# Kernel tuning notes

Measured on AMD Instinct MI355X. Metric: run time of the kernel, lower is better.

## Reference

```python
import jax, jax.numpy as jnp
import numpy as np

R, C = 9, 9  # local window (rows, cols)


def setup_inputs() -> dict:
    key = jax.random.key(0)
    k1, k2, k3, k4, k5 = jax.random.split(key, 5)
    q = jax.random.normal(k1, (8, 256, 128, 128), jnp.float32)      # (B, q_size, H, W)
    c_t = jax.random.normal(k2, (8, 256, 512), jnp.float32)          # (B, T, c_size)
    W_a = jax.random.normal(k3, (512, 256), jnp.float32) * 0.04      # Linear(q_size -> c_size), no bias
    W_p = jax.random.normal(k4, (256, 512), jnp.float32) * 0.04      # Linear(c_size -> p_size)
    V_p = jax.random.normal(k5, (2, 256), jnp.float32) * 0.06        # Linear(p_size -> 2)
    return {"q": q, "c_t": c_t, "W_a": W_a, "W_p": W_p, "V_p": V_p}


def reference(q, c_t, W_a, W_p, V_p):
    B, D, H, W = q.shape
    T = c_t.shape[1]
    S = H  # q.size(2) before padding

    # predictive alignment: p_t = S * sigmoid(V_p(tanh(W_p(c_t))))  -> (B, T, 2)
    p_t = S * jax.nn.sigmoid(jnp.tanh(c_t @ W_p.T) @ V_p.T)

    # pad top/left with NaN, flatten spatial dims
    qp = jnp.pad(q, ((0, 0), (0, 0), (1, 0), (1, 0)), constant_values=jnp.nan)
    rows, cols = H + 1, W + 1
    qf = qp.reshape(B, D, rows * cols).transpose(0, 2, 1)  # (B, rows*cols, D)

    roff = jnp.arange(-(R // 2), (R + 1) // 2)  # R offsets
    coff = jnp.arange(-(C // 2), (C + 1) // 2)  # C offsets
    r = jnp.clip(jnp.round(p_t[..., 0]).astype(jnp.int32)[..., None] + roff + 1, 0, rows) % rows  # (B,T,R)
    c = jnp.clip(jnp.round(p_t[..., 1]).astype(jnp.int32)[..., None] + coff + 1, 0, cols) % cols  # (B,T,C)

    # flat window indices, order i*C + j (matches torch stack order)
    s = (r[..., :, None] * cols + c[..., None, :]).reshape(B, T, R * C)

    # gather windows: (B, T, R*C, D)
    qg = jnp.take_along_axis(qf, s.reshape(B, T * R * C, 1), axis=1).reshape(B, T, R * C, D)
    nan_loc = jnp.isnan(qg[..., 0])                    # (B, T, R*C)
    qg = jnp.where(nan_loc[..., None], 0.0, qg)

    # Gaussian positional weighting
    rexp = -2.0 * ((jnp.clip(r - 1, 0, None).astype(jnp.float32) - p_t[..., 0:1]) / (R // 2)) ** 2
    cexp = -2.0 * ((jnp.clip(c - 1, 0, None).astype(jnp.float32) - p_t[..., 1:2]) / (C // 2)) ** 2
    gauss = jnp.exp((rexp[..., :, None] + cexp[..., None, :]).reshape(B, T, R * C))

    # score: (W_a q) . c_t  -> (B, T, R*C)
    a_t = jnp.einsum('btkd,cd,btc->btk', qg, W_a, c_t)
    a_t = jnp.where(nan_loc, -jnp.inf, a_t)
    W_attn = jax.nn.softmax(a_t, axis=2) * gauss

    out = jnp.einsum('btk,btkd->btd', W_attn, qg)  # (B, T, D)
    return out
```

## Files before the change

kernel.cpp:

```cpp
#include <hip/hip_runtime.h>
#include <math.h>

#define Bq 8
#define Tt 256
#define Dd 256
#define Hh 128
#define Ww 128
#define Cc 512
#define HW (Hh*Ww)
#define NBT (Bq*Tt)

__device__ __forceinline__ float lane_bcast(float x, int l) {
    return __uint_as_float(__builtin_amdgcn_readlane(__float_as_uint(x), l));
}

__global__ __launch_bounds__(256) void transpose_wp(
    const float* __restrict__ W_p, float* __restrict__ WpT)
{
    __shared__ float tile[32][33];
    const int bx = blockIdx.x;
    const int by = blockIdx.y;
    const int lx = threadIdx.x & 31, ly = threadIdx.x >> 5;
#pragma unroll
    for (int j = 0; j < 4; j++) {
        int p = by * 32 + ly + j * 8;
        tile[ly + j * 8][lx] = W_p[(size_t)p * Cc + bx * 32 + lx];
    }
    __syncthreads();
#pragma unroll
    for (int j = 0; j < 4; j++) {
        int c = bx * 32 + ly + j * 8;
        WpT[(size_t)c * 256 + by * 32 + lx] = tile[lx][ly + j * 8];
    }
}

#define TOK 4
__global__ __launch_bounds__(512) void prep_kernel(
    const float* __restrict__ c_t,
    const float* __restrict__ W_a,
    const float* __restrict__ WpT,
    const float* __restrict__ V_p,
    float* __restrict__ u_ws,
    float* __restrict__ p_ws)
{
    __shared__ float y0s[TOK][256];
    __shared__ float y1s[TOK][256];
    const int tid  = threadIdx.x;
    const int o    = tid & 255;
    const int half = tid >> 8;
    const int ln   = tid & 63;
    const int bt0  = blockIdx.x * TOK;

    const float* Wcol = (half ? WpT : W_a) + o;
    const float* ctb  = c_t + (size_t)bt0 * Cc;

    float acc[TOK];
#pragma unroll
    for (int t = 0; t < TOK; t++) acc[t] = 0.f;

    float ctr[TOK], ctn[TOK];
#pragma unroll
    for (int t = 0; t < TOK; t++) ctr[t] = ctb[t * Cc + ln];

#pragma unroll
    for (int c0 = 0; c0 < Cc; c0 += 64) {
        if (c0 + 64 < Cc) {
#pragma unroll
            for (int t = 0; t < TOK; t++) ctn[t] = ctb[t * Cc + c0 + 64 + ln];
        }
#pragma unroll
        for (int cc8 = 0; cc8 < 64; cc8 += 8) {
            float w[8];
#pragma unroll
            for (int j = 0; j < 8; j++)
                w[j] = Wcol[(size_t)(c0 + cc8 + j) * 256];
#pragma unroll
            for (int j = 0; j < 8; j++) {
#pragma unroll
                for (int t = 0; t < TOK; t++)
                    acc[t] = fmaf(lane_bcast(ctr[t], cc8 + j), w[j], acc[t]);
            }
        }
#pragma unroll
        for (int t = 0; t < TOK; t++) ctr[t] = ctn[t];
    }

    if (half == 0) {
#pragma unroll
        for (int t = 0; t < TOK; t++)
            u_ws[(size_t)(bt0 + t) * Dd + o] = acc[t];
    } else {
        float v0 = V_p[o], v1 = V_p[256 + o];
#pragma unroll
        for (int t = 0; t < TOK; t++) {
            float th = tanhf(acc[t]);
            y0s[t][o] = th * v0;
            y1s[t][o] = th * v1;
        }
    }
    __syncthreads();

    const int wv = tid >> 6;
    const int t  = wv & 3;
    const float* ys = (wv < 4) ? &y0s[t][0] : &y1s[t][0];
    float s = ys[ln] + ys[ln + 64] + ys[ln + 128] + ys[ln + 192];
#pragma unroll
    for (int of = 32; of >= 1; of >>= 1) s += __shfl_xor(s, of);
    if (ln == 0)
        p_ws[(size_t)(bt0 + t) * 2 + ((wv < 4) ? 0 : 1)] = 128.f / (1.f + expf(-s));
}

__global__ __launch_bounds__(256) void attn_kernel(
    const float* __restrict__ q,
    const float* __restrict__ u_ws,
    const float* __restrict__ p_ws,
    float* __restrict__ out)
{
    __shared__ __align__(16) _Float16 win[Dd][9][12];
    __shared__ __align__(16) float pacc_s[8][9][12];
    __shared__ float ascore[9][12];
    __shared__ float u_s[Dd];
    __shared__ float w_s[81];
    __shared__ float a_s[81];
    __shared__ float e_s[81];
    __shared__ float rex_s[9], cex_s[9];
    __shared__ int   rr_s[9], cc_s[9];
    __shared__ float m_sh, inv_sh;

    const int tid = threadIdx.x;
    int bt = blockIdx.x;
    bt = ((bt & 7) << 8) | (bt >> 3);
    const int b = bt >> 8;

    u_s[tid] = u_ws[(size_t)bt * Dd + tid];

    {
        float4* wf = (float4*)&win[0][0][0];
        for (int i = tid; i < 3456; i += 256) wf[i] = make_float4(0.f, 0.f, 0.f, 0.f);
        float* pz = &pacc_s[0][0][0];
        for (int i = tid; i < 864; i += 256) pz[i] = 0.f;
    }

    if (tid < 18) {
        int   i = (tid < 9) ? tid : tid - 9;
        float p = p_ws[(size_t)bt * 2 + ((tid < 9) ? 0 : 1)];
        int base = (int)rintf(p);
        int v = base + i - 3;
        v = min(max(v, 0), 129) % 129;
        float cl = (float)max(v - 1, 0);
        float z  = (cl - p) * 0.25f;
        float ex = -2.f * z * z;
        if (tid < 9) { rr_s[i] = v; rex_s[i] = ex; }
        else         { cc_s[i] = v; cex_s[i] = ex; }
    }
    __syncthreads();

    int jc0 = 0, c0 = 1;
#pragma unroll
    for (int j = 8; j >= 0; j--)
        if (cc_s[j] > 0) { jc0 = j; c0 = cc_s[j]; }
    const int cb = min((c0 - 1) & ~3, Ww - 12);
    const int e0 = (c0 - 1) - cb;

    {
        const int g  = tid >> 5;
        const int l5 = tid & 31;
        const bool lact = (l5 < 27);
        const int li = lact ? ((l5 * 171) >> 9) : 0;
        const int lv = l5 - li * 3;
        const int vr = lact ? rr_s[li] : 0;
        const int rowoff = (max(vr, 1) - 1) * Ww + cb + 4 * lv;
        const float* qb = q + (size_t)b * Dd * HW;
        if (lact && vr > 0) {
            float px = 0.f, py = 0.f, pz = 0.f, pw = 0.f;
            for (int dd = 0; dd < Dd; dd += 32) {
                const int d0 = dd + g;
                float4 x0 = *(const float4*)(qb + (size_t)(d0     ) * HW + rowoff);
                float4 x1 = *(const float4*)(qb + (size_t)(d0 +  8) * HW + rowoff);
                float4 x2 = *(const float4*)(qb + (size_t)(d0 + 16) * HW + rowoff);
                float4 x3 = *(const float4*)(qb + (size_t)(d0 + 24) * HW + rowoff);
                float u0 = u_s[d0], u1 = u_s[d0 + 8], u2 = u_s[d0 + 16], u3 = u_s[d0 + 24];
                px = fmaf(x0.x, u0, px); py = fmaf(x0.y, u0, py);
                pz = fmaf(x0.z, u0, pz); pw = fmaf(x0.w, u0, pw);
                px = fmaf(x1.x, u1, px); py = fmaf(x1.y, u1, py);
                pz = fmaf(x1.z, u1, pz); pw = fmaf(x1.w, u1, pw);
                px = fmaf(x2.x, u2, px); py = fmaf(x2.y, u2, py);
                pz = fmaf(x2.z, u2, pz); pw = fmaf(x2.w, u2, pw);
                px = fmaf(x3.x, u3, px); py = fmaf(x3.y, u3, py);
                pz = fmaf(x3.z, u3, pz); pw = fmaf(x3.w, u3, pw);
                union { _Float16 h[4]; uint2 u; } p0, p1, p2, p3;
                p0.h[0] = (_Float16)x0.x; p0.h[1] = (_Float16)x0.y;
                p0.h[2] = (_Float16)x0.z; p0.h[3] = (_Float16)x0.w;
                p1.h[0] = (_Float16)x1.x; p1.h[1] = (_Float16)x1.y;
                p1.h[2] = (_Float16)x1.z; p1.h[3] = (_Float16)x1.w;
                p2.h[0] = (_Float16)x2.x; p2.h[1] = (_Float16)x2.y;
                p2.h[2] = (_Float16)x2.z; p2.h[3] = (_Float16)x2.w;
                p3.h[0] = (_Float16)x3.x; p3.h[1] = (_Float16)x3.y;
                p3.h[2] = (_Float16)x3.z; p3.h[3] = (_Float16)x3.w;
                *(uint2*)&win[d0     ][li][4 * lv] = p0.u;
                *(uint2*)&win[d0 +  8][li][4 * lv] = p1.u;
                *(uint2*)&win[d0 + 16][li][4 * lv] = p2.u;
                *(uint2*)&win[d0 + 24][li][4 * lv] = p3.u;
            }
            *(float4*)&pacc_s[g][li][4 * lv] = make_float4(px, py, pz, pw);
        }
    }
    __syncthreads();

    if (tid < 108) {
        const int li  = tid / 12;
        const int pos = tid - li * 12;
        float s = 0.f;
#pragma unroll
        for (int g = 0; g < 8; g++) s += pacc_s[g][li][pos];
        ascore[li][pos] = s;
    }
    __syncthreads();

    float a_val = -INFINITY;
    bool  valid_k = false;
    if (tid < 81) {
        const int ki = (tid * 57) >> 9;
        const int kj = tid - ki * 9;
        valid_k = (rr_s[ki] > 0) && (cc_s[kj] > 0);
        const int pos = min(max(e0 + kj - jc0, 0), 11);
        a_val = valid_k ? ascore[ki][pos] : -INFINITY;
        a_s[tid] = a_val;
    }
    __syncthreads();

    if (tid < 64) {
        float m = a_s[tid];
        if (tid + 64 < 81) m = fmaxf(m, a_s[tid + 64]);
        for (int o = 32; o >= 1; o >>= 1) m = fmaxf(m, __shfl_xor(m, o));
        if (tid == 0) m_sh = m;
    }
    __syncthreads();
    {
        float e = 0.f;
        if (tid < 81 && valid_k) e = expf(a_val - m_sh);
        if (tid < 81) e_s[tid] = e;
    }
    __syncthreads();
    if (tid < 64) {
        float sv = e_s[tid] + ((tid + 64 < 81) ? e_s[tid + 64] : 0.f);
        for (int o = 32; o >= 1; o >>= 1) sv += __shfl_xor(sv, o);
        if (tid == 0) inv_sh = 1.f / sv;
    }
    __syncthreads();
    if (tid < 81) {
        int i = (tid * 57) >> 9;
        int j = tid - i * 9;
        float g = expf(rex_s[i] + cex_s[j]);
        w_s[tid] = e_s[tid] * inv_sh * g;
    }
    __syncthreads();

    int posj[9];
#pragma unroll
    for (int j = 0; j < 9; j++) posj[j] = min(max(e0 + j - jc0, 0), 11);
    const _Float16* wd = &win[tid][0][0];
    float acc = 0.f;
#pragma unroll
    for (int k = 0; k < 81; k++) {
        const int ki = k / 9, kj = k % 9;
        acc = fmaf(w_s[k], (float)wd[ki * 12 + posj[kj]], acc);
    }
    out[(size_t)bt * Dd + tid] = acc;
}

extern "C" void kernel_launch(void* const* d_in, const int* in_sizes, int n_in,
                              void* d_out, int out_size, void* d_ws, size_t ws_size,
                              hipStream_t stream) {
    const float* q   = (const float*)d_in[0];
    const float* c_t = (const float*)d_in[1];
    const float* W_a = (const float*)d_in[2];
    const float* W_p = (const float*)d_in[3];
    const float* V_p = (const float*)d_in[4];
    float* out  = (float*)d_out;
    float* u_ws = (float*)d_ws;
    float* p_ws = u_ws + (size_t)NBT * Dd;
    float* WpT  = p_ws + (size_t)NBT * 2;

    transpose_wp<<<dim3(16, 8), 256, 0, stream>>>(W_p, WpT);
    prep_kernel<<<NBT / TOK, 512, 0, stream>>>(c_t, W_a, WpT, V_p, u_ws, p_ws);
    attn_kernel<<<NBT, 256, 0, stream>>>(q, u_ws, p_ws, out);
}
```

Baseline: 264.0 us.

## Double-buffer window loads, drop shared-memory zeroing, and batch more tokens in prep

The window gather loop now prefetches the next group of four float4 loads while the current group is being processed, and the u values are read into registers up front. The zero-fill of the window and partial-score shared buffers is removed, and rows that fall on the NaN pad are now loaded from a clamped row instead of skipped, which saves a barrier-free clearing pass. In the prep kernel each block now handles 8 tokens, and each wave reduces both alignment outputs. The risk is correctness: padded-row entries and unwritten columns are no longer zero, so this relies on later masking, and the double buffer adds register pressure.

```diff
diff --git a/kernel.cpp b/kernel.cpp
--- a/kernel.cpp
+++ b/kernel.cpp
@@ -34,7 +34,7 @@
     }
 }
 
-#define TOK 4
+#define TOK 8
 __global__ __launch_bounds__(512) void prep_kernel(
     const float* __restrict__ c_t,
     const float* __restrict__ W_a,
@@ -101,13 +101,17 @@
     __syncthreads();
 
     const int wv = tid >> 6;
-    const int t  = wv & 3;
-    const float* ys = (wv < 4) ? &y0s[t][0] : &y1s[t][0];
-    float s = ys[ln] + ys[ln + 64] + ys[ln + 128] + ys[ln + 192];
-#pragma unroll
-    for (int of = 32; of >= 1; of >>= 1) s += __shfl_xor(s, of);
-    if (ln == 0)
-        p_ws[(size_t)(bt0 + t) * 2 + ((wv < 4) ? 0 : 1)] = 128.f / (1.f + expf(-s));
+    float s0 = y0s[wv][ln] + y0s[wv][ln + 64] + y0s[wv][ln + 128] + y0s[wv][ln + 192];
+    float s1 = y1s[wv][ln] + y1s[wv][ln + 64] + y1s[wv][ln + 128] + y1s[wv][ln + 192];
+#pragma unroll
+    for (int of = 32; of >= 1; of >>= 1) {
+        s0 += __shfl_xor(s0, of);
+        s1 += __shfl_xor(s1, of);
+    }
+    if (ln == 0) {
+        p_ws[(size_t)(bt0 + wv) * 2 + 0] = 128.f / (1.f + expf(-s0));
+        p_ws[(size_t)(bt0 + wv) * 2 + 1] = 128.f / (1.f + expf(-s1));
+    }
 }
 
 __global__ __launch_bounds__(256) void attn_kernel(
@@ -134,13 +138,6 @@
 
     u_s[tid] = u_ws[(size_t)bt * Dd + tid];
 
-    {
-        float4* wf = (float4*)&win[0][0][0];
-        for (int i = tid; i < 3456; i += 256) wf[i] = make_float4(0.f, 0.f, 0.f, 0.f);
-        float* pz = &pacc_s[0][0][0];
-        for (int i = tid; i < 864; i += 256) pz[i] = 0.f;
-    }
-
     if (tid < 18) {
         int   i = (tid < 9) ? tid : tid - 9;
         float p = p_ws[(size_t)bt * 2 + ((tid < 9) ? 0 : 1)];
@@ -168,39 +165,42 @@
         const bool lact = (l5 < 27);
         const int li = lact ? ((l5 * 171) >> 9) : 0;
         const int lv = l5 - li * 3;
-        const int vr = lact ? rr_s[li] : 0;
+        const int vr = lact ? rr_s[li] : 1;
         const int rowoff = (max(vr, 1) - 1) * Ww + cb + 4 * lv;
-        const float* qb = q + (size_t)b * Dd * HW;
-        if (lact && vr > 0) {
+        const float* qp = q + (size_t)b * Dd * HW + rowoff;
+
+        if (lact) {
+            float u_r[32];
+#pragma unroll
+            for (int m = 0; m < 32; m++) u_r[m] = u_s[g + 8 * m];
+
             float px = 0.f, py = 0.f, pz = 0.f, pw = 0.f;
-            for (int dd = 0; dd < Dd; dd += 32) {
-                const int d0 = dd + g;
-                float4 x0 = *(const float4*)(qb + (size_t)(d0     ) * HW + rowoff);
-                float4 x1 = *(const float4*)(qb + (size_t)(d0 +  8) * HW + rowoff);
-                float4 x2 = *(const float4*)(qb + (size_t)(d0 + 16) * HW + rowoff);
-                float4 x3 = *(const float4*)(qb + (size_t)(d0 + 24) * HW + rowoff);
-                float u0 = u_s[d0], u1 = u_s[d0 + 8], u2 = u_s[d0 + 16], u3 = u_s[d0 + 24];
-                px = fmaf(x0.x, u0, px); py = fmaf(x0.y, u0, py);
-                pz = fmaf(x0.z, u0, pz); pw = fmaf(x0.w, u0, pw);
-                px = fmaf(x1.x, u1, px); py = fmaf(x1.y, u1, py);
-                pz = fmaf(x1.z, u1, pz); pw = fmaf(x1.w, u1, pw);
-                px = fmaf(x2.x, u2, px); py = fmaf(x2.y, u2, py);
-                pz = fmaf(x2.z, u2, pz); pw = fmaf(x2.w, u2, pw);
-                px = fmaf(x3.x, u3, px); py = fmaf(x3.y, u3, py);
-                pz = fmaf(x3.z, u3, pz); pw = fmaf(x3.w, u3, pw);
-                union { _Float16 h[4]; uint2 u; } p0, p1, p2, p3;
-                p0.h[0] = (_Float16)x0.x; p0.h[1] = (_Float16)x0.y;
-                p0.h[2] = (_Float16)x0.z; p0.h[3] = (_Float16)x0.w;
-                p1.h[0] = (_Float16)x1.x; p1.h[1] = (_Float16)x1.y;
-                p1.h[2] = (_Float16)x1.z; p1.h[3] = (_Float16)x1.w;
-                p2.h[0] = (_Float16)x2.x; p2.h[1] = (_Float16)x2.y;
-                p2.h[2] = (_Float16)x2.z; p2.h[3] = (_Float16)x2.w;
-                p3.h[0] = (_Float16)x3.x; p3.h[1] = (_Float16)x3.y;
-                p3.h[2] = (_Float16)x3.z; p3.h[3] = (_Float16)x3.w;
-                *(uint2*)&win[d0     ][li][4 * lv] = p0.u;
-                *(uint2*)&win[d0 +  8][li][4 * lv] = p1.u;
-                *(uint2*)&win[d0 + 16][li][4 * lv] = p2.u;
-                *(uint2*)&win[d0 + 24][li][4 * lv] = p3.u;
+            float4 xb[2][4];
+#pragma unroll
+            for (int mm = 0; mm < 4; mm++)
+                xb[0][mm] = *(const float4*)(qp + (size_t)(g + 8 * mm) * HW);
+
+            for (int it = 0; it < 8; it++) {
+                const int cur = it & 1;
+                if (it < 7) {
+#pragma unroll
+                    for (int mm = 0; mm < 4; mm++)
+                        xb[cur ^ 1][mm] = *(const float4*)
+                            (qp + (size_t)(g + 8 * (4 * (it + 1) + mm)) * HW);
+                }
+#pragma unroll
+                for (int mm = 0; mm < 4; mm++) {
+                    const int m  = 4 * it + mm;
+                    const int d0 = g + 8 * m;
+                    float4 x = xb[cur][mm];
+                    float  u = u_r[m];
+                    px = fmaf(x.x, u, px); py = fmaf(x.y, u, py);
+                    pz = fmaf(x.z, u, pz); pw = fmaf(x.w, u, pw);
+                    union { _Float16 h[4]; uint2 uu; } pk;
+                    pk.h[0] = (_Float16)x.x; pk.h[1] = (_Float16)x.y;
+                    pk.h[2] = (_Float16)x.z; pk.h[3] = (_Float16)x.w;
+                    *(uint2*)&win[d0][li][4 * lv] = pk.uu;
+                }
             }
             *(float4*)&pacc_s[g][li][4 * lv] = make_float4(px, py, pz, pw);
         }
```

After: 263.0 us. Within noise of the previous version (-0.4%).
